# Kernel tuning notes

Measured on AMD Instinct MI355X. Metric: run time of the kernel, lower is better.

## Reference

```python
import jax, jax.numpy as jnp
import numpy as np

SM_SCALE = 0.08838834764831845  # 1/sqrt(128)
SLIDING_WINDOW = 128
N_TOKENS, N_HEADS, Q_MULT, D_HEAD = 2048, 8, 4, 128


def setup_inputs() -> dict:
    key = jax.random.key(0)
    k1, k2, k3, k4 = jax.random.split(key, 4)
    Q = jax.random.normal(k1, (N_TOKENS, N_HEADS, Q_MULT, D_HEAD), dtype=jnp.float32)
    K = jax.random.normal(k2, (N_TOKENS, N_HEADS, D_HEAD), dtype=jnp.float32)
    V = jax.random.normal(k3, (N_TOKENS, N_HEADS, D_HEAD), dtype=jnp.float32)
    S = jax.random.normal(k4, (N_HEADS * Q_MULT,), dtype=jnp.float32)
    return {"Q": Q, "K": K, "V": V, "S": S}


def _build_mask(n_tokens, sliding_window, dtype):
    q_idx = jnp.arange(n_tokens)[:, None]
    k_idx = jnp.arange(n_tokens)[None, :]
    # causal: disallow k > q; sliding window: disallow k <= q - sliding_window
    disallowed = k_idx > q_idx
    if sliding_window > 0:
        disallowed = disallowed | (k_idx <= q_idx - sliding_window)
    return jnp.where(disallowed, jnp.array(-jnp.inf, dtype), jnp.array(0.0, dtype))


def reference(Q, K, V, S):
    n_tokens, n_heads, q_mult, d_head = Q.shape
    mask = _build_mask(n_tokens, SLIDING_WINDOW, Q.dtype)  # (T, T)
    # scores: (h, m, q, k)
    QK = jnp.einsum('qhmd,khd->hmqk', Q, K) * SM_SCALE
    QK = QK + mask[None, None, :, :]
    # append per-(head, q_mult) sink logit as an extra key column
    sink = jnp.broadcast_to(S.reshape(n_heads, q_mult, 1, 1),
                            (n_heads, q_mult, n_tokens, 1))
    QK = jnp.concatenate([QK, sink], axis=-1)  # (h, m, q, k+1)
    W = jax.nn.softmax(QK, axis=-1)[..., :-1]  # drop sink column
    attn = jnp.einsum('hmqk,khd->qhmd', W, V)
    return attn.reshape(n_tokens, n_heads * q_mult * d_head)
```

## Files before the change

### kernel.cpp

```cpp
#include <hip/hip_runtime.h>
#include <cstdint>

#define T_TOK 2048
#define NH 8
#define QM 4
#define DH 128
#define BQ 32
#define QS 136
#define PS 40
#define SM_SCALE 0.08838834764831845f

typedef __attribute__((ext_vector_type(8))) short short8v;
typedef __attribute__((ext_vector_type(4))) short short4v;
typedef __attribute__((ext_vector_type(2))) short short2v;
typedef __attribute__((ext_vector_type(4))) float floatx4;

static __device__ __forceinline__ short f2bf(float x) {
  union { float f; unsigned u; } v; v.f = x;
  return (short)((v.u + 0x7fffu + ((v.u >> 16) & 1u)) >> 16);
}

__global__ __launch_bounds__(256)
void preconvert(const float* __restrict__ K, const float* __restrict__ V,
                short* __restrict__ Kf, short* __restrict__ Vf) {
  __shared__ __align__(16) short lt[64][136];
  const int b = blockIdx.x, t = threadIdx.x;
  const int isK = b < 256 ? 1 : 0;
  const int bb = isK ? b : b - 256;
  const int h = bb & 7, t0 = (bb >> 3) << 6;
  const float* src0 = isK ? K : V;

  {
    const int tt = t >> 2, d0 = (t & 3) * 32;
    const float* src = src0 + ((size_t)(t0 + tt) * NH + h) * DH + d0;
#pragma unroll
    for (int u = 0; u < 8; ++u) {
      float4 x = *(const float4*)(src + 4 * u);
      short4v s4;
      s4[0] = f2bf(x.x); s4[1] = f2bf(x.y); s4[2] = f2bf(x.z); s4[3] = f2bf(x.w);
      *(short4v*)(&lt[tt][d0 + 4 * u]) = s4;
    }
  }
  __syncthreads();

  const int lane = t & 63, quad = (t >> 4) & 3, l16 = t & 15;
  if (isK) {
    const int s = t >> 6;
#pragma unroll
    for (int T = 0; T < 4; ++T) {
      short8v o = *(const short8v*)(&lt[T * 16 + l16][quad * 8 + s * 32]);
      short* dst = Kf + ((((size_t)h * 128 + (t0 >> 4) + T) * 4 + s) * 64 + lane) * 8;
      *(short8v*)dst = o;
    }
  } else {
    const int grp = t >> 6;
#pragma unroll
    for (int w = 0; w < 4; ++w) {
      const int u = grp + 4 * w;
      const int cp = u >> 3, nt = u & 7;
      short8v o;
#pragma unroll
      for (int j = 0; j < 8; ++j) {
        const int key = quad * 4 + (j >> 1) + 16 * (j & 1);
        o[j] = lt[cp * 32 + key][l16 + 16 * nt];
      }
      short* dst = Vf + ((((size_t)h * 64 + (t0 >> 5) + cp) * 8 + nt) * 64 + lane) * 8;
      *(short8v*)dst = o;
    }
  }
}

__global__ __launch_bounds__(256, 2)
void attn_fwd(const float* __restrict__ Qp, const short* __restrict__ Kf,
              const short* __restrict__ Vf, const float* __restrict__ Sp,
              float* __restrict__ Op) {
  __shared__ __align__(16) short q_s[128 * QS];
  __shared__ __align__(16) short p_s[128 * PS];

  const int t    = threadIdx.x;
  const int lane = t & 63;
  const int wv   = t >> 6;
  const int quad = lane >> 4;
  const int l16  = lane & 15;

  const int bx = blockIdx.x;
  const int h  = bx & 7;
  const int q0 = (bx >> 3) * BQ;
  int lo0 = q0 > 127 ? q0 - 127 : 0;
  lo0 &= ~31;
  const int nk  = q0 + BQ - lo0;
  const int nch = (nk + 31) >> 5;

  {
    const float* qsrc = Qp + ((size_t)q0 * 32 + h * 4) * 128;
#pragma unroll
    for (int p = 0; p < 16; ++p) {
      const int g = t + p * 256;
      const int seg = g >> 7, w = g & 127;
      const float4 x = *(const float4*)(qsrc + (size_t)seg * 4096 + w * 4);
      short4v s4;
      s4[0] = f2bf(x.x); s4[1] = f2bf(x.y); s4[2] = f2bf(x.z); s4[3] = f2bf(x.w);
      *(short4v*)(&q_s[(seg * 4 + (w >> 5)) * QS + (w & 31) * 4]) = s4;
    }
  }
  __syncthreads();

  short8v qf[2][4];
#pragma unroll
  for (int T = 0; T < 2; ++T)
#pragma unroll
    for (int s = 0; s < 4; ++s)
      qf[T][s] = *(const short8v*)(&q_s[(wv * 32 + T * 16 + l16) * QS + quad * 8 + 32 * s]);

  float dn[2][4];
#pragma unroll
  for (int T = 0; T < 2; ++T)
#pragma unroll
    for (int r = 0; r < 4; ++r) dn[T][r] = 0.f;
  floatx4 oacc[2][8];
#pragma unroll
  for (int T = 0; T < 2; ++T)
#pragma unroll
    for (int nt = 0; nt < 8; ++nt) oacc[T][nt] = (floatx4)0.0f;

  const short* kfb = Kf + (((size_t)h * 128 + (lo0 >> 4)) * 4 * 64 + lane) * 8;
  const short* vfb = Vf + (((size_t)h * 64 + (lo0 >> 5)) * 8 * 64 + lane) * 8;

  for (int c = 0; c < nch; ++c) {
    const int kb = lo0 + c * 32;
    const short* kf = kfb + (size_t)c * 4096;
    const short* vf = vfb + (size_t)c * 4096;

    floatx4 sc[2][2];
    sc[0][0] = (floatx4)0.0f; sc[0][1] = (floatx4)0.0f;
    sc[1][0] = (floatx4)0.0f; sc[1][1] = (floatx4)0.0f;
#pragma unroll
    for (int s = 0; s < 4; ++s) {
      short8v k0 = *(const short8v*)(kf + s * 512);
      short8v k1 = *(const short8v*)(kf + 2048 + s * 512);
      sc[0][0] = __builtin_amdgcn_mfma_f32_16x16x32_bf16(qf[0][s], k0, sc[0][0], 0, 0, 0);
      sc[0][1] = __builtin_amdgcn_mfma_f32_16x16x32_bf16(qf[0][s], k1, sc[0][1], 0, 0, 0);
      sc[1][0] = __builtin_amdgcn_mfma_f32_16x16x32_bf16(qf[1][s], k0, sc[1][0], 0, 0, 0);
      sc[1][1] = __builtin_amdgcn_mfma_f32_16x16x32_bf16(qf[1][s], k1, sc[1][1], 0, 0, 0);
    }

    const int k0i = kb + l16, k1i = kb + 16 + l16;
#pragma unroll
    for (int T = 0; T < 2; ++T) {
      const int qc = q0 + 8 * wv + 4 * T + quad;
      const bool ok0 = (k0i <= qc) && (k0i > qc - 128);
      const bool ok1 = (k1i <= qc) && (k1i > qc - 128);
      const int Rb = wv * 32 + T * 16 + quad * 4;
#pragma unroll
      for (int r = 0; r < 4; ++r) {
        float e0 = ok0 ? __expf(sc[T][0][r] * SM_SCALE) : 0.f;
        float e1 = ok1 ? __expf(sc[T][1][r] * SM_SCALE) : 0.f;
        dn[T][r] += e0 + e1;
        short2v p2; p2[0] = f2bf(e0); p2[1] = f2bf(e1);
        *(short2v*)(&p_s[(Rb + r) * PS + 2 * l16]) = p2;
      }
    }

    short8v pf0 = *(const short8v*)(&p_s[(wv * 32 + l16) * PS + quad * 8]);
    short8v pf1 = *(const short8v*)(&p_s[(wv * 32 + 16 + l16) * PS + quad * 8]);
#pragma unroll
    for (int nt = 0; nt < 8; ++nt) {
      short8v vfr = *(const short8v*)(vf + nt * 512);
      oacc[0][nt] = __builtin_amdgcn_mfma_f32_16x16x32_bf16(pf0, vfr, oacc[0][nt], 0, 0, 0);
      oacc[1][nt] = __builtin_amdgcn_mfma_f32_16x16x32_bf16(pf1, vfr, oacc[1][nt], 0, 0, 0);
    }
  }

#pragma unroll
  for (int T = 0; T < 2; ++T) {
    const int qc = q0 + 8 * wv + 4 * T + quad;
#pragma unroll
    for (int r = 0; r < 4; ++r) {
      float s = dn[T][r];
#pragma unroll
      for (int mm = 1; mm <= 8; mm <<= 1) s += __shfl_xor(s, mm);
      const float total = s + __expf(Sp[h * QM + r]);
      const float rd = 1.0f / total;
      float* ob = Op + (size_t)qc * 4096 + (h * 4 + r) * 128 + l16;
#pragma unroll
      for (int nt = 0; nt < 8; ++nt) ob[nt * 16] = oacc[T][nt][r] * rd;
    }
  }
}

extern "C" void kernel_launch(void* const* d_in, const int* in_sizes, int n_in,
                              void* d_out, int out_size, void* d_ws, size_t ws_size,
                              hipStream_t stream) {
  const float* Q = (const float*)d_in[0];
  const float* K = (const float*)d_in[1];
  const float* V = (const float*)d_in[2];
  const float* S = (const float*)d_in[3];
  float* O = (float*)d_out;
  short* Kf = (short*)d_ws;
  short* Vf = Kf + (size_t)8 * 128 * 4 * 64 * 8;

  preconvert<<<dim3(512), dim3(256), 0, stream>>>(K, V, Kf, Vf);
  const int grid = (T_TOK / BQ) * NH;
  attn_fwd<<<dim3(grid), dim3(256), 0, stream>>>(Q, Kf, Vf, S, O);
}
```

Measured before the change: 109.0 us.

## Prefetch K/V fragments into registers and split V conversion into direct-gather blocks

The attention kernel now loads the next chunk's K fragments into registers while the current chunk's scores are computed, and issues all V fragment loads at the top of each chunk, before the QK MFMAs. This hides global-memory latency behind the matrix math. The preconvert kernel gets 768 blocks: V blocks each handle 32 keys and gather and convert V directly from global memory without going through LDS. The gather issues strided scalar loads, which may coalesce poorly, and the extra register-held fragments raise register pressure at 2 blocks per CU.

```diff
diff --git a/kernel.cpp b/kernel.cpp
--- a/kernel.cpp
+++ b/kernel.cpp
@@ -25,26 +25,22 @@
                 short* __restrict__ Kf, short* __restrict__ Vf) {
   __shared__ __align__(16) short lt[64][136];
   const int b = blockIdx.x, t = threadIdx.x;
-  const int isK = b < 256 ? 1 : 0;
-  const int bb = isK ? b : b - 256;
-  const int h = bb & 7, t0 = (bb >> 3) << 6;
-  const float* src0 = isK ? K : V;
-
-  {
-    const int tt = t >> 2, d0 = (t & 3) * 32;
-    const float* src = src0 + ((size_t)(t0 + tt) * NH + h) * DH + d0;
-#pragma unroll
-    for (int u = 0; u < 8; ++u) {
-      float4 x = *(const float4*)(src + 4 * u);
-      short4v s4;
-      s4[0] = f2bf(x.x); s4[1] = f2bf(x.y); s4[2] = f2bf(x.z); s4[3] = f2bf(x.w);
-      *(short4v*)(&lt[tt][d0 + 4 * u]) = s4;
-    }
-  }
-  __syncthreads();
-
   const int lane = t & 63, quad = (t >> 4) & 3, l16 = t & 15;
-  if (isK) {
+
+  if (b < 256) {
+    const int h = b & 7, t0 = (b >> 3) << 6;
+    {
+      const int tt = t >> 2, d0 = (t & 3) * 32;
+      const float* src = K + ((size_t)(t0 + tt) * NH + h) * DH + d0;
+#pragma unroll
+      for (int u = 0; u < 8; ++u) {
+        float4 x = *(const float4*)(src + 4 * u);
+        short4v s4;
+        s4[0] = f2bf(x.x); s4[1] = f2bf(x.y); s4[2] = f2bf(x.z); s4[3] = f2bf(x.w);
+        *(short4v*)(&lt[tt][d0 + 4 * u]) = s4;
+      }
+    }
+    __syncthreads();
     const int s = t >> 6;
 #pragma unroll
     for (int T = 0; T < 4; ++T) {
@@ -53,19 +49,20 @@
       *(short8v*)dst = o;
     }
   } else {
-    const int grp = t >> 6;
-#pragma unroll
-    for (int w = 0; w < 4; ++w) {
-      const int u = grp + 4 * w;
-      const int cp = u >> 3, nt = u & 7;
+    const int bb = b - 256;
+    const int h = bb & 7, c = bb >> 3;
+    const int u = t >> 6;
+    const float* vb = V + (size_t)(c * 32) * (NH * DH) + h * DH;
+#pragma unroll
+    for (int p = 0; p < 2; ++p) {
+      const int nt = u + 4 * p;
       short8v o;
 #pragma unroll
       for (int j = 0; j < 8; ++j) {
         const int key = quad * 4 + (j >> 1) + 16 * (j & 1);
-        o[j] = lt[cp * 32 + key][l16 + 16 * nt];
-      }
-      short* dst = Vf + ((((size_t)h * 64 + (t0 >> 5) + cp) * 8 + nt) * 64 + lane) * 8;
-      *(short8v*)dst = o;
+        o[j] = f2bf(vb[(size_t)key * (NH * DH) + l16 + 16 * nt]);
+      }
+      *(short8v*)(Vf + ((((size_t)h * 64 + c) * 8 + nt) * 64 + lane) * 8) = o;
     }
   }
 }
@@ -126,22 +123,39 @@
   const short* kfb = Kf + (((size_t)h * 128 + (lo0 >> 4)) * 4 * 64 + lane) * 8;
   const short* vfb = Vf + (((size_t)h * 64 + (lo0 >> 5)) * 8 * 64 + lane) * 8;
 
+  short8v kr[8];
+#pragma unroll
+  for (int s = 0; s < 4; ++s) {
+    kr[s]     = *(const short8v*)(kfb + s * 512);
+    kr[4 + s] = *(const short8v*)(kfb + 2048 + s * 512);
+  }
+
   for (int c = 0; c < nch; ++c) {
     const int kb = lo0 + c * 32;
-    const short* kf = kfb + (size_t)c * 4096;
     const short* vf = vfb + (size_t)c * 4096;
+
+    short8v vr[8];
+#pragma unroll
+    for (int nt = 0; nt < 8; ++nt) vr[nt] = *(const short8v*)(vf + nt * 512);
 
     floatx4 sc[2][2];
     sc[0][0] = (floatx4)0.0f; sc[0][1] = (floatx4)0.0f;
     sc[1][0] = (floatx4)0.0f; sc[1][1] = (floatx4)0.0f;
 #pragma unroll
     for (int s = 0; s < 4; ++s) {
-      short8v k0 = *(const short8v*)(kf + s * 512);
-      short8v k1 = *(const short8v*)(kf + 2048 + s * 512);
-      sc[0][0] = __builtin_amdgcn_mfma_f32_16x16x32_bf16(qf[0][s], k0, sc[0][0], 0, 0, 0);
-      sc[0][1] = __builtin_amdgcn_mfma_f32_16x16x32_bf16(qf[0][s], k1, sc[0][1], 0, 0, 0);
-      sc[1][0] = __builtin_amdgcn_mfma_f32_16x16x32_bf16(qf[1][s], k0, sc[1][0], 0, 0, 0);
-      sc[1][1] = __builtin_amdgcn_mfma_f32_16x16x32_bf16(qf[1][s], k1, sc[1][1], 0, 0, 0);
+      sc[0][0] = __builtin_amdgcn_mfma_f32_16x16x32_bf16(qf[0][s], kr[s],     sc[0][0], 0, 0, 0);
+      sc[0][1] = __builtin_amdgcn_mfma_f32_16x16x32_bf16(qf[0][s], kr[4 + s], sc[0][1], 0, 0, 0);
+      sc[1][0] = __builtin_amdgcn_mfma_f32_16x16x32_bf16(qf[1][s], kr[s],     sc[1][0], 0, 0, 0);
+      sc[1][1] = __builtin_amdgcn_mfma_f32_16x16x32_bf16(qf[1][s], kr[4 + s], sc[1][1], 0, 0, 0);
+    }
+
+    if (c + 1 < nch) {
+      const short* kfn = kfb + (size_t)(c + 1) * 4096;
+#pragma unroll
+      for (int s = 0; s < 4; ++s) {
+        kr[s]     = *(const short8v*)(kfn + s * 512);
+        kr[4 + s] = *(const short8v*)(kfn + 2048 + s * 512);
+      }
     }
 
     const int k0i = kb + l16, k1i = kb + 16 + l16;
@@ -165,9 +179,8 @@
     short8v pf1 = *(const short8v*)(&p_s[(wv * 32 + 16 + l16) * PS + quad * 8]);
 #pragma unroll
     for (int nt = 0; nt < 8; ++nt) {
-      short8v vfr = *(const short8v*)(vf + nt * 512);
-      oacc[0][nt] = __builtin_amdgcn_mfma_f32_16x16x32_bf16(pf0, vfr, oacc[0][nt], 0, 0, 0);
-      oacc[1][nt] = __builtin_amdgcn_mfma_f32_16x16x32_bf16(pf1, vfr, oacc[1][nt], 0, 0, 0);
+      oacc[0][nt] = __builtin_amdgcn_mfma_f32_16x16x32_bf16(pf0, vr[nt], oacc[0][nt], 0, 0, 0);
+      oacc[1][nt] = __builtin_amdgcn_mfma_f32_16x16x32_bf16(pf1, vr[nt], oacc[1][nt], 0, 0, 0);
     }
   }
 
@@ -199,7 +212,7 @@
   short* Kf = (short*)d_ws;
   short* Vf = Kf + (size_t)8 * 128 * 4 * 64 * 8;
 
-  preconvert<<<dim3(512), dim3(256), 0, stream>>>(K, V, Kf, Vf);
+  preconvert<<<dim3(768), dim3(256), 0, stream>>>(K, V, Kf, Vf);
   const int grid = (T_TOK / BQ) * NH;
   attn_fwd<<<dim3(grid), dim3(256), 0, stream>>>(Q, Kf, Vf, S, O);
 }
```

Result: slower. 111.3 us (+2.2%).
